# Performance work log

Hardware: AMD Instinct MI355X
Metric: run time of the kernel (lower is better)

Reference implementation:

```python
import jax, jax.numpy as jnp
import numpy as np

D = 128  # head dim

def setup_inputs() -> dict:
    key = jax.random.key(0)
    k1, k2, k3, k4, k5 = jax.random.split(key, 5)
    B, N, M, C1, C2 = 4, 4096, 4096, 1024, 1024
    x = jax.random.normal(k1, (B, N, C1), dtype=jnp.float32)
    y = jax.random.normal(k2, (B, M, C2), dtype=jnp.float32)
    # Linear(c, d, bias=False): out = inp @ W where W is [c, d]
    Wq = jax.random.normal(k3, (C1, D), dtype=jnp.float32) / np.sqrt(C1)
    Wk = jax.random.normal(k4, (C2, D), dtype=jnp.float32) / np.sqrt(C2)
    Wv = jax.random.normal(k5, (C2, D), dtype=jnp.float32) / np.sqrt(C2)
    return {"x": x, "y": y, "Wq": Wq, "Wk": Wk, "Wv": Wv}

def reference(x, y, Wq, Wk, Wv):
    q = x @ Wq                               # [B, N, d]
    k = y @ Wk                               # [B, M, d]
    v = y @ Wv                               # [B, M, d]
    scale = 1.0 / jnp.sqrt(jnp.asarray(D, dtype=q.dtype))
    a = jnp.einsum('bnd,bmd->bnm', q, k) * scale
    a = jax.nn.softmax(a, axis=-1)           # softmax FIRST
    a = jnp.triu(a, k=1)                     # post-softmax causal mask (keeps strict upper)
    out = jnp.einsum('bnm,bmd->bnd', a, v)   # [B, N, d]
    return out
```

## Files before the change

kernel.cpp:

```cpp
#include <hip/hip_runtime.h>
#include <hip/hip_bf16.h>
#include <stdint.h>


typedef __attribute__((ext_vector_type(8))) __bf16    bf16x8;
typedef __attribute__((ext_vector_type(4))) float     floatx4;
typedef __attribute__((ext_vector_type(8))) uint16_t  u16x8;
typedef __attribute__((ext_vector_type(4))) uint32_t  u32x4;

#define DEVFN __device__ __forceinline__

DEVFN uint16_t f32_to_bf16(float f) {
  uint32_t u = __builtin_bit_cast(uint32_t, f);
  u += 0x7FFFu + ((u >> 16) & 1u);
  return (uint16_t)(u >> 16);
}

DEVFN uint32_t bcast(float f) { return __builtin_bit_cast(uint32_t, f); }

DEVFN uint32_t pack2_bf16(float a, float b) {
  return ((bcast(a) + 0x8000u) >> 16) | ((bcast(b) + 0x8000u) & 0xFFFF0000u);
}

DEVFN u32x4 pack_bf16_8(float4 a0, float4 a1) {
  u32x4 o;
  o[0] = pack2_bf16(a0.x, a0.y);
  o[1] = pack2_bf16(a0.z, a0.w);
  o[2] = pack2_bf16(a1.x, a1.y);
  o[3] = pack2_bf16(a1.z, a1.w);
  return o;
}

__global__ __launch_bounds__(256) void wt_kernel(
    const float* __restrict__ Wq, const float* __restrict__ Wk,
    const float* __restrict__ Wv, uint16_t* __restrict__ wt) {
  int tid = blockIdx.x * 256 + threadIdx.x;
  int mat = tid >> 14;
  int rem = tid & 16383;
  int n  = rem & 127;
  int k0 = rem >> 7;
  const float* W = (mat == 0) ? Wq : ((mat == 1) ? Wk : Wv);
  u16x8 v;
#pragma unroll
  for (int j = 0; j < 8; ++j) v[j] = f32_to_bf16(W[(k0 * 8 + j) * 128 + n]);
  *(u16x8*)&wt[mat * (128 * 1024) + n * 1024 + k0 * 8] = v;
}

__global__ __launch_bounds__(256) void qkv_kernel(
    const float* __restrict__ x, const float* __restrict__ y,
    const uint16_t* __restrict__ wt, uint16_t* __restrict__ q,
    uint16_t* __restrict__ k, uint16_t* __restrict__ vt) {
  constexpr int LDT = 72;
  constexpr int ABUF = 128 * LDT;
  __shared__ __align__(16) uint16_t sA[2 * ABUF];
  __shared__ __align__(16) uint16_t sW[2 * ABUF];
  const int t = threadIdx.x;
  const int mat = blockIdx.y, rt = blockIdx.x;
  const float* A = (mat == 0) ? x : y;
  const uint16_t* Wt = wt + mat * (128 * 1024);
  const int lane = t & 63, wv = t >> 6;
  const int cidx = lane & 15, quad = lane >> 4;
  const int sr = t >> 3;
  const int sc = (t & 7) * 8;
  const int Arow0 = rt * 128;

  floatx4 acc[2][8];
#pragma unroll
  for (int rg = 0; rg < 2; ++rg)
#pragma unroll
    for (int ng = 0; ng < 8; ++ng) acc[rg][ng] = (floatx4){0.f, 0.f, 0.f, 0.f};

  float4 a0r[4], a1r[4];
  u16x8 wr[4];
#pragma unroll
  for (int u = 0; u < 4; ++u) {
    int row = u * 32 + sr;
    const float* ap = &A[(size_t)(Arow0 + row) * 1024 + sc];
    a0r[u] = *(const float4*)ap;
    a1r[u] = *(const float4*)(ap + 4);
    wr[u]  = *(const u16x8*)&Wt[row * 1024 + sc];
  }
#pragma unroll
  for (int u = 0; u < 4; ++u) {
    int row = u * 32 + sr;
    *(u32x4*)&sA[row * LDT + sc] = pack_bf16_8(a0r[u], a1r[u]);
    *(u16x8*)&sW[row * LDT + sc] = wr[u];
  }
  __syncthreads();

  for (int kt = 0; kt < 16; ++kt) {
    const int cur = kt & 1, nxt = cur ^ 1;
    if (kt < 15) {
      const int kc = (kt + 1) * 64;
#pragma unroll
      for (int u = 0; u < 4; ++u) {
        int row = u * 32 + sr;
        const float* ap = &A[(size_t)(Arow0 + row) * 1024 + kc + sc];
        a0r[u] = *(const float4*)ap;
        a1r[u] = *(const float4*)(ap + 4);
        wr[u]  = *(const u16x8*)&Wt[row * 1024 + kc + sc];
      }
    }
    bf16x8 af[2][2];
#pragma unroll
    for (int rg = 0; rg < 2; ++rg)
#pragma unroll
      for (int ks = 0; ks < 2; ++ks)
        af[rg][ks] = *(const bf16x8*)
            &sA[cur * ABUF + (wv * 32 + rg * 16 + cidx) * LDT + ks * 32 + quad * 8];
#pragma unroll
    for (int ng = 0; ng < 8; ++ng) {
      bf16x8 b0 = *(const bf16x8*)&sW[cur * ABUF + (ng * 16 + cidx) * LDT + quad * 8];
      bf16x8 b1 = *(const bf16x8*)&sW[cur * ABUF + (ng * 16 + cidx) * LDT + 32 + quad * 8];
#pragma unroll
      for (int rg = 0; rg < 2; ++rg) {
        acc[rg][ng] = __builtin_amdgcn_mfma_f32_16x16x32_bf16(af[rg][0], b0, acc[rg][ng], 0, 0, 0);
        acc[rg][ng] = __builtin_amdgcn_mfma_f32_16x16x32_bf16(af[rg][1], b1, acc[rg][ng], 0, 0, 0);
      }
    }
    if (kt < 15) {
#pragma unroll
      for (int u = 0; u < 4; ++u) {
        int row = u * 32 + sr;
        *(u32x4*)&sA[nxt * ABUF + row * LDT + sc] = pack_bf16_8(a0r[u], a1r[u]);
        *(u16x8*)&sW[nxt * ABUF + row * LDT + sc] = wr[u];
      }
    }
    __syncthreads();
  }

  if (mat < 2) {
    uint16_t* outp = (mat == 0) ? q : k;
#pragma unroll
    for (int rg = 0; rg < 2; ++rg)
#pragma unroll
      for (int r = 0; r < 4; ++r) {
        int row = Arow0 + wv * 32 + rg * 16 + quad * 4 + r;
#pragma unroll
        for (int ng = 0; ng < 8; ++ng)
          outp[row * 128 + ng * 16 + cidx] = f32_to_bf16(acc[rg][ng][r]);
      }
  } else {
    int bq = rt >> 5;
    int mbase = (rt & 31) * 128;
#pragma unroll
    for (int rg = 0; rg < 2; ++rg)
#pragma unroll
      for (int r = 0; r < 4; ++r) {
        int m = mbase + wv * 32 + rg * 16 + quad * 4 + r;
#pragma unroll
        for (int ng = 0; ng < 8; ++ng)
          vt[(size_t)(bq * 128 + ng * 16 + cidx) * 4096 + m] = f32_to_bf16(acc[rg][ng][r]);
      }
  }
}

__global__ __launch_bounds__(256, 4) void attn_kernel(
    const uint16_t* __restrict__ q, const uint16_t* __restrict__ k,
    const uint16_t* __restrict__ vt, float* __restrict__ opart,
    float* __restrict__ lpart, int mlen, int iters) {
  constexpr int LDK = 136, LDV = 72;
  __shared__ __align__(16) uint16_t sK[64 * LDK];
  __shared__ __align__(16) uint16_t sV[128 * LDV];
  const int t = threadIdx.x;
  const int lane = t & 63, wv = t >> 6;
  const int cidx = lane & 15, quad = lane >> 4;
  const int qt = blockIdx.x, h = blockIdx.y, b = blockIdx.z;
  const int qmin = qt * 64 + wv * 16;
  const int mbase = h * mlen;

  const uint16_t* qb = q + (size_t)(b * 4096) * 128;
  const uint16_t* kb = k + (size_t)(b * 4096) * 128;
  const uint16_t* vb = vt + (size_t)(b * 128) * 4096;

  const float SC = 0.12751744610657223f;

  bf16x8 qf[4];
#pragma unroll
  for (int ks = 0; ks < 4; ++ks)
    qf[ks] = *(const bf16x8*)&qb[(qmin + cidx) * 128 + ks * 32 + quad * 8];

  floatx4 O[8];
#pragma unroll
  for (int dg = 0; dg < 8; ++dg) O[dg] = (floatx4){0.f, 0.f, 0.f, 0.f};
  float lsum = 0.f;

  const int krow = t >> 4, kcol = (t & 15) * 8;
  const int vrow = t >> 3, vcol = (t & 7) * 8;

  for (int it = 0; it < iters; ++it) {
    const int m0 = mbase + it * 64;
    u16x8 kr[4], vr[4];
#pragma unroll
    for (int u = 0; u < 4; ++u) {
      kr[u] = *(const u16x8*)&kb[(m0 + u * 16 + krow) * 128 + kcol];
      vr[u] = *(const u16x8*)&vb[(size_t)(u * 32 + vrow) * 4096 + m0 + vcol];
    }
#pragma unroll
    for (int u = 0; u < 4; ++u) {
      *(u16x8*)&sK[(u * 16 + krow) * LDK + kcol] = kr[u];
      *(u16x8*)&sV[(u * 32 + vrow) * LDV + vcol] = vr[u];
    }
    __syncthreads();

    floatx4 accST[4];
#pragma unroll
    for (int ng = 0; ng < 4; ++ng) accST[ng] = (floatx4){0.f, 0.f, 0.f, 0.f};
#pragma unroll
    for (int ks = 0; ks < 4; ++ks) {
      bf16x8 qv = qf[ks];
#pragma unroll
      for (int ng = 0; ng < 4; ++ng) {
        bf16x8 kf = *(const bf16x8*)
            &sK[(ng * 16 + cidx) * LDK + ks * 32 + quad * 8];
        accST[ng] = __builtin_amdgcn_mfma_f32_16x16x32_bf16(kf, qv, accST[ng], 0, 0, 0);
      }
    }

    float p[4][4];
#pragma unroll
    for (int ng = 0; ng < 4; ++ng)
#pragma unroll
      for (int r = 0; r < 4; ++r) {
        p[ng][r] = exp2f(accST[ng][r] * SC);
        lsum += p[ng][r];
      }

    if (m0 + 63 > qmin) {
      if (m0 < qmin + 16) {
#pragma unroll
        for (int ng = 0; ng < 4; ++ng)
#pragma unroll
          for (int r = 0; r < 4; ++r) {
            int m = m0 + ng * 16 + quad * 4 + r;
            int n = qmin + cidx;
            if (m <= n) p[ng][r] = 0.f;
          }
      }
      uint32_t pk[4][2];
#pragma unroll
      for (int ng = 0; ng < 4; ++ng) {
        pk[ng][0] = pack2_bf16(p[ng][0], p[ng][1]);
        pk[ng][1] = pack2_bf16(p[ng][2], p[ng][3]);
      }
#pragma unroll
      for (int ks = 0; ks < 2; ++ks) {
        u32x4 pbw;
#pragma unroll
        for (int j2 = 0; j2 < 4; ++j2) {
          int lr = ((quad & 1) << 3) + 2 * j2;
          int srcl = ((lr >> 2) << 4) + cidx;
          uint32_t lo = (uint32_t)__shfl((int)pk[2 * ks][j2 & 1], srcl);
          uint32_t hi = (uint32_t)__shfl((int)pk[2 * ks + 1][j2 & 1], srcl);
          pbw[j2] = (quad & 2) ? hi : lo;
        }
        bf16x8 pbv = __builtin_bit_cast(bf16x8, pbw);
#pragma unroll
        for (int dg = 0; dg < 8; ++dg) {
          bf16x8 vf = *(const bf16x8*)
              &sV[(dg * 16 + cidx) * LDV + ks * 32 + quad * 8];
          O[dg] = __builtin_amdgcn_mfma_f32_16x16x32_bf16(vf, pbv, O[dg], 0, 0, 0);
        }
      }
    }
    __syncthreads();
  }

  lsum += __shfl_xor(lsum, 16);
  lsum += __shfl_xor(lsum, 32);

  const int n = qmin + cidx;
  float* op = opart + ((size_t)h * 16384 + b * 4096 + n) * 128;
#pragma unroll
  for (int dg = 0; dg < 8; ++dg)
    *(float4*)&op[dg * 16 + quad * 4] = __builtin_bit_cast(float4, O[dg]);
  if (quad == 0) lpart[h * 16384 + b * 4096 + n] = lsum;
}

__global__ __launch_bounds__(256) void combine_kernel(
    const float* __restrict__ opart, const float* __restrict__ lpart,
    float* __restrict__ out, int hcount) {
  size_t i = (size_t)blockIdx.x * 256 + threadIdx.x;
  size_t e = i * 4;
  int row = (int)(e >> 7);
  float4 acc = {0.f, 0.f, 0.f, 0.f};
  float l = 0.f;
  for (int h = 0; h < hcount; ++h) {
    float4 ov = *(const float4*)&opart[(size_t)h * 2097152 + e];
    acc.x += ov.x; acc.y += ov.y; acc.z += ov.z; acc.w += ov.w;
    l += lpart[h * 16384 + row];
  }
  float inv = 1.0f / l;
  float4 o;
  o.x = acc.x * inv; o.y = acc.y * inv; o.z = acc.z * inv; o.w = acc.w * inv;
  *(float4*)&out[e] = o;
}

extern "C" void kernel_launch(void* const* d_in, const int* in_sizes, int n_in,
                              void* d_out, int out_size, void* d_ws, size_t ws_size,
                              hipStream_t stream) {
  const float* x  = (const float*)d_in[0];
  const float* y  = (const float*)d_in[1];
  const float* Wq = (const float*)d_in[2];
  const float* Wk = (const float*)d_in[3];
  const float* Wv = (const float*)d_in[4];
  uint16_t* ws = (uint16_t*)d_ws;
  uint16_t* wt = ws;
  uint16_t* q  = ws + 393216;
  uint16_t* k  = q + 2097152;
  uint16_t* vt = k + 2097152;
  float* opart = (float*)((char*)d_ws + 13369344);
  int hcount = (ws_size >= (size_t)13369344 + 4 * 8454144) ? 4 : 2;
  float* lpart = opart + (size_t)hcount * 2097152;
  float* o = (float*)d_out;
  int mlen = 4096 / hcount, iters = mlen / 64;

  hipLaunchKernelGGL(wt_kernel,      dim3(192),            dim3(256), 0, stream, Wq, Wk, Wv, wt);
  hipLaunchKernelGGL(qkv_kernel,     dim3(128, 3),         dim3(256), 0, stream, x, y, wt, q, k, vt);
  hipLaunchKernelGGL(attn_kernel,    dim3(64, hcount, 4),  dim3(256), 0, stream, q, k, vt, opart, lpart, mlen, iters);
  hipLaunchKernelGGL(combine_kernel, dim3(2048),           dim3(256), 0, stream, opart, lpart, o, hcount);
}
```

Baseline: 240.7 us.

## Double-buffer K/V tiles via direct global-to-LDS loads with XOR swizzle

The attention kernel now loads K and V tiles straight from global memory into LDS using global_load_lds, with two LDS buffers so the next tile is fetched while the current one is computed. Padded LDS layouts are replaced by XOR-swizzled layouts to avoid bank conflicts, and launch bounds drop from 4 to 2 blocks per CU to fit the doubled LDS. The aim is to hide global load latency and skip the register staging round trip, at the cost of lower occupancy. Only one __syncthreads per iteration remains, which may race with the prefetch into the buffer just read.

```diff
diff --git a/kernel.cpp b/kernel.cpp
--- a/kernel.cpp
+++ b/kernel.cpp
@@ -29,6 +29,12 @@
   o[2] = pack2_bf16(a1.x, a1.y);
   o[3] = pack2_bf16(a1.z, a1.w);
   return o;
+}
+
+DEVFN void gl2lds16(const void* g, void* l) {
+  __builtin_amdgcn_global_load_lds(
+      (const __attribute__((address_space(1))) void*)g,
+      (__attribute__((address_space(3))) void*)l, 16, 0, 0);
 }
 
 __global__ __launch_bounds__(256) void wt_kernel(
@@ -155,13 +161,13 @@
   }
 }
 
-__global__ __launch_bounds__(256, 4) void attn_kernel(
+__global__ __launch_bounds__(256, 2) void attn_kernel(
     const uint16_t* __restrict__ q, const uint16_t* __restrict__ k,
     const uint16_t* __restrict__ vt, float* __restrict__ opart,
     float* __restrict__ lpart, int mlen, int iters) {
-  constexpr int LDK = 136, LDV = 72;
-  __shared__ __align__(16) uint16_t sK[64 * LDK];
-  __shared__ __align__(16) uint16_t sV[128 * LDV];
+  constexpr int KB = 16384, VB = 16384;
+  __shared__ __align__(16) uint8_t sK[2 * KB];
+  __shared__ __align__(16) uint8_t sV[2 * VB];
   const int t = threadIdx.x;
   const int lane = t & 63, wv = t >> 6;
   const int cidx = lane & 15, quad = lane >> 4;
@@ -170,10 +176,23 @@
   const int mbase = h * mlen;
 
   const uint16_t* qb = q + (size_t)(b * 4096) * 128;
-  const uint16_t* kb = k + (size_t)(b * 4096) * 128;
-  const uint16_t* vb = vt + (size_t)(b * 128) * 4096;
+  const uint8_t* kb = (const uint8_t*)(k + (size_t)(b * 4096) * 128);
+  const uint8_t* vb = (const uint8_t*)(vt + (size_t)(b * 128) * 4096);
 
   const float SC = 0.12751744610657223f;
+
+  int kOffL[4], vOffL[4], kLds[4], vLds[4];
+#pragma unroll
+  for (int u = 0; u < 4; ++u) {
+    int r  = wv * 16 + u * 4 + (lane >> 4);
+    int g  = (lane & 15) ^ (r & 15);
+    kOffL[u] = r * 256 + g * 16;
+    kLds[u]  = (wv * 16 + u * 4) * 256;
+    int rv = wv * 32 + u * 8 + (lane >> 3);
+    int gv = (lane & 7) ^ (rv & 7);
+    vOffL[u] = rv * 8192 + gv * 16;
+    vLds[u]  = (wv * 32 + u * 8) * 128;
+  }
 
   bf16x8 qf[4];
 #pragma unroll
@@ -185,23 +204,24 @@
   for (int dg = 0; dg < 8; ++dg) O[dg] = (floatx4){0.f, 0.f, 0.f, 0.f};
   float lsum = 0.f;
 
-  const int krow = t >> 4, kcol = (t & 15) * 8;
-  const int vrow = t >> 3, vcol = (t & 7) * 8;
+#pragma unroll
+  for (int u = 0; u < 4; ++u) {
+    gl2lds16(kb + (size_t)mbase * 256 + kOffL[u], sK + kLds[u]);
+    gl2lds16(vb + (size_t)mbase * 2 + vOffL[u], sV + vLds[u]);
+  }
+  __syncthreads();
 
   for (int it = 0; it < iters; ++it) {
     const int m0 = mbase + it * 64;
-    u16x8 kr[4], vr[4];
-#pragma unroll
-    for (int u = 0; u < 4; ++u) {
-      kr[u] = *(const u16x8*)&kb[(m0 + u * 16 + krow) * 128 + kcol];
-      vr[u] = *(const u16x8*)&vb[(size_t)(u * 32 + vrow) * 4096 + m0 + vcol];
-    }
-#pragma unroll
-    for (int u = 0; u < 4; ++u) {
-      *(u16x8*)&sK[(u * 16 + krow) * LDK + kcol] = kr[u];
-      *(u16x8*)&sV[(u * 32 + vrow) * LDV + vcol] = vr[u];
-    }
-    __syncthreads();
+    const int cur = it & 1, nxt = cur ^ 1;
+    if (it + 1 < iters) {
+      const int m1 = m0 + 64;
+#pragma unroll
+      for (int u = 0; u < 4; ++u) {
+        gl2lds16(kb + (size_t)m1 * 256 + kOffL[u], sK + nxt * KB + kLds[u]);
+        gl2lds16(vb + (size_t)m1 * 2 + vOffL[u], sV + nxt * VB + vLds[u]);
+      }
+    }
 
     floatx4 accST[4];
 #pragma unroll
@@ -212,7 +232,7 @@
 #pragma unroll
       for (int ng = 0; ng < 4; ++ng) {
         bf16x8 kf = *(const bf16x8*)
-            &sK[(ng * 16 + cidx) * LDK + ks * 32 + quad * 8];
+            (sK + cur * KB + (ng * 16 + cidx) * 256 + ((ks * 4 + quad) ^ cidx) * 16);
         accST[ng] = __builtin_amdgcn_mfma_f32_16x16x32_bf16(kf, qv, accST[ng], 0, 0, 0);
       }
     }
@@ -258,7 +278,8 @@
 #pragma unroll
         for (int dg = 0; dg < 8; ++dg) {
           bf16x8 vf = *(const bf16x8*)
-              &sV[(dg * 16 + cidx) * LDV + ks * 32 + quad * 8];
+              (sV + cur * VB + (dg * 16 + cidx) * 128 +
+               (((ks * 4 + quad) ^ cidx) & 7) * 16);
           O[dg] = __builtin_amdgcn_mfma_f32_16x16x32_bf16(vf, pbv, O[dg], 0, 0, 0);
         }
       }
```

After: 245.3 us. Within noise of the previous version (+1.9%).
